# Optimization experiments

Hardware: AMD Instinct MI355X
Metric: run time of the kernel (lower is better)

The kernel has to match this reference:

```python
import jax, jax.numpy as jnp
import numpy as np

EPS_NORM = 1e-12
BN_EPS = 1e-5

def _l2norm(x, axis=-1):
    n = jnp.sqrt(jnp.sum(x * x, axis=axis, keepdims=True))
    return x / jnp.maximum(n, EPS_NORM)

def setup_inputs() -> dict:
    key = jax.random.key(0)
    ks = jax.random.split(key, 16)
    B, C, H, W, K = 32, 256, 64, 64, 5
    supp_feat = jax.random.normal(ks[0], (B, C, H, W), dtype=jnp.float32)
    supp_mask = (jax.random.uniform(ks[1], (B, 1, H, W)) > 0.5).astype(jnp.float32)
    part_queries = 0.02 * jax.random.normal(ks[2], (1, K, C), dtype=jnp.float32)
    temperature = jnp.array([0.1], dtype=jnp.float32)
    margin = jnp.array([0.15], dtype=jnp.float32)
    q_w = jax.random.normal(ks[3], (C, C), dtype=jnp.float32) / np.sqrt(C)  # 1x1 conv, no bias
    bn_w = 1.0 + 0.1 * jax.random.normal(ks[4], (C,), dtype=jnp.float32)
    bn_b = 0.1 * jax.random.normal(ks[5], (C,), dtype=jnp.float32)
    bn_mean = 0.1 * jax.random.normal(ks[6], (C,), dtype=jnp.float32)
    bn_var = 0.5 + jax.random.uniform(ks[7], (C,), dtype=jnp.float32)
    k_w = jax.random.normal(ks[8], (C, C), dtype=jnp.float32) / np.sqrt(C)
    k_b = 0.01 * jax.random.normal(ks[9], (C,), dtype=jnp.float32)
    v_w = jax.random.normal(ks[10], (C, C), dtype=jnp.float32) / np.sqrt(C)
    v_b = 0.01 * jax.random.normal(ks[11], (C,), dtype=jnp.float32)
    out_w = jax.random.normal(ks[12], (C, C), dtype=jnp.float32) / np.sqrt(C)
    out_b = 0.01 * jax.random.normal(ks[13], (C,), dtype=jnp.float32)
    gamma = jnp.array([0.1], dtype=jnp.float32)  # nonzero so the refine branch contributes
    return {"supp_feat": supp_feat, "supp_mask": supp_mask, "part_queries": part_queries,
            "temperature": temperature, "margin": margin, "q_w": q_w, "bn_w": bn_w,
            "bn_b": bn_b, "bn_mean": bn_mean, "bn_var": bn_var, "k_w": k_w, "k_b": k_b,
            "v_w": v_w, "v_b": v_b, "out_w": out_w, "out_b": out_b, "gamma": gamma}

def reference(supp_feat, supp_mask, part_queries, temperature, margin, q_w, bn_w, bn_b,
              bn_mean, bn_var, k_w, k_b, v_w, v_b, out_w, out_b, gamma):
    B, C, H, W = supp_feat.shape
    K = part_queries.shape[1]
    flat_mask = supp_mask.reshape(B, -1)                       # [B, HW]
    flat_feat = jnp.swapaxes(supp_feat.reshape(B, C, -1), 1, 2)  # [B, HW, C]
    queries_norm = _l2norm(part_queries)[0]                    # [K, C]
    feat_norm = _l2norm(flat_feat)                             # [B, HW, C]
    temp = jnp.maximum(temperature, 0.01)[0]
    sim = jnp.einsum('kc,bnc->bkn', queries_norm, feat_norm) / temp  # [B, K, HW]
    sim = jnp.where(flat_mask[:, None, :] > 0, sim, -jnp.inf)
    attn = jnp.nan_to_num(jax.nn.softmax(sim, axis=-1), nan=0.0)
    part_tokens = jnp.einsum('bkn,bnc->bkc', attn, flat_feat)  # [B, K, C]
    # diversity loss
    nt = _l2norm(part_tokens)
    cos = jnp.einsum('bkc,bjc->bkj', nt, nt) * (1.0 - jnp.eye(K, dtype=supp_feat.dtype))
    m = jnp.clip(margin, 0.0, 0.5)[0]
    div_loss = jnp.maximum(cos - m, 0.0).sum() / (B * K * (K - 1) + 1e-5)
    # refine attention
    q = jnp.einsum('oc,bchw->bohw', q_w, supp_feat)            # 1x1 conv, no bias
    scale = bn_w / jnp.sqrt(bn_var + BN_EPS)
    q = q * scale[None, :, None, None] + (bn_b - bn_mean * scale)[None, :, None, None]
    Q = jnp.swapaxes(q.reshape(B, C, -1), 1, 2)                # [B, HW, C]
    Kt = part_tokens @ k_w.T + k_b                             # [B, K, C]
    Vt = part_tokens @ v_w.T + v_b
    refine = jax.nn.softmax(jnp.einsum('bnc,bkc->bnk', Q, Kt) / (C ** 0.5), axis=-1)
    attn_out = jnp.einsum('bnk,bkc->bnc', refine, Vt)          # [B, HW, C]
    attn_out = jnp.swapaxes(attn_out, 1, 2).reshape(B, C, H, W)
    attn_out = jnp.einsum('oc,bchw->bohw', out_w, attn_out) + out_b[None, :, None, None]
    enhanced = supp_feat + gamma[0] * attn_out
    return (enhanced, div_loss, part_tokens)
```

## Files before the change

kernel.cpp:

```cpp
#include <hip/hip_runtime.h>
#include <hip/hip_bf16.h>
#include <math.h>

#define B_  32
#define C_  256
#define HW_ 4096
#define K_  5
#define P_  128
#define NT_ 32
#define PS_ 68
#define FS_ 66

typedef __hip_bfloat16 bf16;
typedef unsigned int u32;
typedef __attribute__((ext_vector_type(8))) short bf16x8;
typedef __attribute__((ext_vector_type(4))) float f32x4;

template<bool BF>
__device__ inline float LD(const void* p, size_t i) {
    if (BF) return __bfloat162float(((const bf16*)p)[i]);
    return ((const float*)p)[i];
}
template<bool BF>
__device__ inline void ST(void* p, size_t i, float v) {
    if (BF) ((bf16*)p)[i] = __float2bfloat16(v);
    else    ((float*)p)[i] = v;
}
template<bool BF>
__device__ inline float4 LD4(const void* p, size_t i) {
    if (BF) {
        ushort4 u = *(const ushort4*)((const unsigned short*)p + i);
        float4 r;
        r.x = __uint_as_float(((u32)u.x) << 16);
        r.y = __uint_as_float(((u32)u.y) << 16);
        r.z = __uint_as_float(((u32)u.z) << 16);
        r.w = __uint_as_float(((u32)u.w) << 16);
        return r;
    }
    return *(const float4*)((const float*)p + i);
}
__device__ inline u32 packbf2(float a, float b) {
    bf16 x = __float2bfloat16(a), y = __float2bfloat16(b);
    return (((u32)*(unsigned short*)&y) << 16) | (u32)(*(unsigned short*)&x);
}
__device__ inline float lo16f(u32 u) { return __uint_as_float(u << 16); }
__device__ inline float hi16f(u32 u) { return __uint_as_float(u & 0xffff0000u); }

__device__ int detect_bf(const void* feat, int* cntL) {
    int t = threadIdx.x;
    if (t == 0) *cntL = 0;
    __syncthreads();
    const unsigned short* u = (const unsigned short*)feat;
    float v = __uint_as_float(((u32)u[t]) << 16);
    float a = fabsf(v);
    int local = (a >= 1e-4f && a <= 100.f) ? 1 : 0;
    for (int o = 32; o > 0; o >>= 1) local += __shfl_down(local, o, 64);
    if ((t & 63) == 0) atomicAdd(cntL, local);
    __syncthreads();
    return (*cntL > (int)(3u * blockDim.x / 4u)) ? 1 : 0;
}

__device__ inline float blk_sum(float v, float* sh) {
    for (int o = 32; o > 0; o >>= 1) v += __shfl_down(v, o, 64);
    int w = threadIdx.x >> 6;
    __syncthreads();
    if ((threadIdx.x & 63) == 0) sh[w] = v;
    __syncthreads();
    return sh[0] + sh[1] + sh[2] + sh[3];
}

template<bool BF>
__device__ void simpt_body(const void* feat, const void* mask, const void* temp,
                           const void* pq, float* ptp, float* mz, float* smem) {
    u32*   featB = (u32*)smem;
    float* red   = smem + 17408;
    u32*   wB    = (u32*)red;
    float* qL    = smem + 17408 + 1536;
    float* simL  = qL;
    float* sc    = qL + 1280;
    int t = threadIdx.x, lane = t & 63, q = t >> 6;
    int b = blockIdx.y, tile = blockIdx.x;

    if (q < K_) {
        float4 v = LD4<BF>(pq, (size_t)q * C_ + lane * 4);
        float ss = v.x * v.x + v.y * v.y + v.z * v.z + v.w * v.w;
        for (int o = 32; o > 0; o >>= 1) ss += __shfl_xor(ss, o, 64);
        float inv = 1.0f / fmaxf(sqrtf(ss), 1e-12f);
        *(float4*)(qL + q * C_ + lane * 4) =
            make_float4(v.x * inv, v.y * inv, v.z * inv, v.w * inv);
    }
    if (t == 0) sc[0] = 1.0f / fmaxf(LD<BF>(temp, 0), 0.01f);
    __syncthreads();

    int c0 = q * 32, half = lane >> 5, lm = lane & 31;
    float sa[4] = {0.f, 0.f, 0.f, 0.f};
    float da[K_][4];
    #pragma unroll
    for (int k = 0; k < K_; k++)
        #pragma unroll
        for (int i = 0; i < 4; i++) da[k][i] = 0.f;
    size_t gbase = (size_t)b * C_ * HW_ + (size_t)tile * P_ + lm * 4;
    #pragma unroll
    for (int j = 0; j < 16; j++) {
        int c = c0 + 2 * j + half;
        float4 f = LD4<BF>(feat, gbase + (size_t)c * HW_);
        sa[0] += f.x * f.x; sa[1] += f.y * f.y; sa[2] += f.z * f.z; sa[3] += f.w * f.w;
        #pragma unroll
        for (int k = 0; k < K_; k++) {
            float qv = qL[k * C_ + c];
            da[k][0] += f.x * qv; da[k][1] += f.y * qv;
            da[k][2] += f.z * qv; da[k][3] += f.w * qv;
        }
        *(uint2*)&featB[c * PS_ + 2 * lm] =
            make_uint2(packbf2(f.x, f.y), packbf2(f.z, f.w));
    }
    #pragma unroll
    for (int i = 0; i < 4; i++) sa[i] += __shfl_down(sa[i], 32, 64);
    #pragma unroll
    for (int k = 0; k < K_; k++)
        #pragma unroll
        for (int i = 0; i < 4; i++) da[k][i] += __shfl_down(da[k][i], 32, 64);

    float4 mpre = make_float4(0.f, 0.f, 0.f, 0.f);
    if (t < 160) mpre = LD4<BF>(mask, (size_t)b * HW_ + tile * P_ + (t & 31) * 4);
    float tinv = sc[0];
    #pragma unroll
    for (int r = 0; r < 4; r++) {
        if (lane < 32) {
            red[0 * 256 + q * 32 + lane] = sa[r];
            #pragma unroll
            for (int k = 0; k < K_; k++) red[(1 + k) * 256 + q * 32 + lane] = da[k][r];
        }
        __syncthreads();
        if (t < 160) {
            int kk = t >> 5, m = t & 31, n = 4 * m + r;
            float ssum = 0.f, dsum = 0.f;
            #pragma unroll
            for (int g = 0; g < 8; g++) {
                ssum += red[0 * 256 + g * 32 + m];
                dsum += red[(1 + kk) * 256 + g * 32 + m];
            }
            float mval = (r == 0) ? mpre.x : (r == 1) ? mpre.y : (r == 2) ? mpre.z : mpre.w;
            simL[kk * P_ + n] = (mval > 0.f)
                ? dsum * (tinv / fmaxf(sqrtf(ssum), 1e-12f)) : -INFINITY;
        }
        __syncthreads();
    }

    if (q < K_) {
        float s0 = simL[q * P_ + 2 * lane], s1 = simL[q * P_ + 2 * lane + 1];
        float m = fmaxf(s0, s1);
        for (int o = 32; o > 0; o >>= 1) m = fmaxf(m, __shfl_xor(m, o, 64));
        float e0 = (s0 == -INFINITY) ? 0.f : __expf(s0 - m);
        float e1 = (s1 == -INFINITY) ? 0.f : __expf(s1 - m);
        float z = e0 + e1;
        for (int o = 32; o > 0; o >>= 1) z += __shfl_xor(z, o, 64);
        wB[q * PS_ + lane] = packbf2(e0, e1);
        if (lane == 0) {
            size_t mzb = ((size_t)(b * NT_ + tile) * K_ + q) * 2;
            mz[mzb] = m; mz[mzb + 1] = z;
        }
    }
    __syncthreads();

    int r16 = lane & 15, g = lane >> 4;
    size_t pb = (size_t)(b * NT_ + tile) * (K_ * C_);
    #pragma unroll
    for (int sub = 0; sub < 2; sub++) {
        int ctile = q * 32 + sub * 16;
        f32x4 acc = {0.f, 0.f, 0.f, 0.f};
        #pragma unroll
        for (int s = 0; s < 4; s++) {
            bf16x8 a = *(const bf16x8*)(featB + (ctile + r16) * PS_ + 16 * s + 4 * g);
            bf16x8 bb = *(const bf16x8*)(wB + r16 * PS_ + 16 * s + 4 * g);
            acc = __builtin_amdgcn_mfma_f32_16x16x32_bf16(a, bb, acc, 0, 0, 0);
        }
        if (r16 < K_) {
            #pragma unroll
            for (int r = 0; r < 4; r++)
                ptp[pb + (size_t)r16 * C_ + ctile + 4 * g + r] = acc[r];
        }
    }
}
__global__ __launch_bounds__(512, 4) void k_simpt(const void* feat, const void* mask,
                                                  const void* temp, const void* pq,
                                                  float* ptp, float* mz) {
    __shared__ __attribute__((aligned(16))) float smem[20232];
    __shared__ int cnt;
    int flg = detect_bf(feat, &cnt);
    if (flg) simpt_body<true >(feat, mask, temp, pq, ptp, mz, smem);
    else     simpt_body<false>(feat, mask, temp, pq, ptp, mz, smem);
}

__device__ inline float merge_one(const float* ptp, const float* mz,
                                  int b, int kk, int c) {
    float M = -INFINITY;
    #pragma unroll 8
    for (int tl = 0; tl < NT_; tl++)
        M = fmaxf(M, mz[((size_t)(b * NT_ + tl) * K_ + kk) * 2]);
    float Zs = 0.f, acc = 0.f;
    #pragma unroll 8
    for (int tl = 0; tl < NT_; tl++) {
        size_t mzb = ((size_t)(b * NT_ + tl) * K_ + kk) * 2;
        float m_t = mz[mzb], z_t = mz[mzb + 1];
        float s = (m_t == -INFINITY) ? 0.f : __expf(m_t - M);
        Zs += z_t * s;
        acc += ptp[(size_t)(b * NT_ + tl) * (K_ * C_) + kk * C_ + c] * s;
    }
    return (Zs > 0.f) ? acc / Zs : 0.f;
}
template<bool BF>
__device__ void prep_part(const void* qw, const void* kw, const void* kb,
                          const void* vw, const void* vb, const void* ow,
                          const void* bnw, const void* bnb, const void* bnm,
                          const void* bnv, float ptv, int bk,
                          float* W2, float* b2, float* OV, float* pt, float* smem) {
    float* ptL = smem;
    float* KtL = smem + 256;
    float* VtL = smem + 512;
    float* sh  = smem + 768;
    int t = threadIdx.x;
    ptL[t] = ptv;
    pt[(size_t)bk * C_ + t] = ptv;
    __syncthreads();
    float kt = LD<BF>(kb, t), vt = LD<BF>(vb, t);
    for (int c = 0; c < C_; c += 4) {
        float4 p4 = *(float4*)(ptL + c);
        float4 kw4 = LD4<BF>(kw, (size_t)t * C_ + c);
        float4 vw4 = LD4<BF>(vw, (size_t)t * C_ + c);
        kt += kw4.x * p4.x + kw4.y * p4.y + kw4.z * p4.z + kw4.w * p4.w;
        vt += vw4.x * p4.x + vw4.y * p4.y + vw4.z * p4.z + vw4.w * p4.w;
    }
    float scale = LD<BF>(bnw, t) * rsqrtf(LD<BF>(bnv, t) + 1e-5f);
    float shift = LD<BF>(bnb, t) - LD<BF>(bnm, t) * scale;
    KtL[t] = kt * scale;
    VtL[t] = vt;
    float bpart = kt * shift;
    __syncthreads();
    float ov = 0;
    for (int c = 0; c < C_; c += 4) {
        float4 v4 = *(float4*)(VtL + c);
        float4 ow4 = LD4<BF>(ow, (size_t)t * C_ + c);
        ov += ow4.x * v4.x + ow4.y * v4.y + ow4.z * v4.z + ow4.w * v4.w;
    }
    OV[(size_t)bk * C_ + t] = ov;
    float w2 = 0;
    for (int o = 0; o < C_; o++) w2 += KtL[o] * LD<BF>(qw, (size_t)o * C_ + t);
    W2[(size_t)bk * C_ + t] = w2 * (1.0f / 16.0f);
    float bs = blk_sum(bpart, sh);
    if (t == 0) b2[bk] = bs * (1.0f / 16.0f);
}
template<bool BF>
__device__ void div_part(const float* ptp, const float* mz, const void* margin,
                         float* divpart, float* smem) {
    float* ptL = smem;
    float* rn  = smem + K_ * C_;
    float* sh  = rn + 8;
    int b = blockIdx.x - B_ * K_, t = threadIdx.x;
    for (int kk = 0; kk < K_; kk++) ptL[kk * C_ + t] = merge_one(ptp, mz, b, kk, t);
    __syncthreads();
    for (int k = 0; k < K_; k++) {
        float v = ptL[k * C_ + t];
        float s = blk_sum(v * v, sh);
        if (t == 0) rn[k] = 1.0f / fmaxf(sqrtf(s), 1e-12f);
    }
    __syncthreads();
    float m = LD<BF>(margin, 0);
    m = fminf(fmaxf(m, 0.f), 0.5f);
    int p = t >> 3, g = t & 7;
    float contrib = 0.f;
    if (p < K_ * K_) {
        int k = p / K_, j = p % K_;
        float d = 0;
        for (int c = g; c < C_; c += 8) d += ptL[k * C_ + c] * ptL[j * C_ + c];
        d += __shfl_down(d, 4, 8);
        d += __shfl_down(d, 2, 8);
        d += __shfl_down(d, 1, 8);
        if (g == 0 && k != j) contrib = fmaxf(d * rn[k] * rn[j] - m, 0.f);
    }
    float s = blk_sum(contrib, sh);
    if (t == 0) divpart[b] = s;
}
template<bool BF>
__device__ void mergeprep_body(const void* qw, const void* kw, const void* kb,
                               const void* vw, const void* vb, const void* ow,
                               const void* bnw, const void* bnb, const void* bnm,
                               const void* bnv, const void* margin,
                               const float* ptp, const float* mz,
                               float* W2, float* b2, float* OV, float* pt,
                               float* divpart, float* smem) {
    int bid = blockIdx.x, t = threadIdx.x;
    if (bid < B_ * K_) {
        int b = bid / K_, kk = bid % K_;
        float ptv = merge_one(ptp, mz, b, kk, t);
        prep_part<BF>(qw, kw, kb, vw, vb, ow, bnw, bnb, bnm, bnv,
                      ptv, bid, W2, b2, OV, pt, smem);
    } else {
        div_part<BF>(ptp, mz, margin, divpart, smem);
    }
}
__global__ void k_mergeprep(const void* feat, const void* qw, const void* kw,
                            const void* kb, const void* vw, const void* vb,
                            const void* ow, const void* bnw, const void* bnb,
                            const void* bnm, const void* bnv, const void* margin,
                            const float* ptp, const float* mz,
                            float* W2, float* b2, float* OV, float* pt, float* divpart) {
    __shared__ __attribute__((aligned(16))) float smem[K_ * C_ + 16];
    __shared__ int cnt;
    int flg = detect_bf(feat, &cnt);
    if (flg) mergeprep_body<true >(qw, kw, kb, vw, vb, ow, bnw, bnb, bnm, bnv, margin,
                                   ptp, mz, W2, b2, OV, pt, divpart, smem);
    else     mergeprep_body<false>(qw, kw, kb, vw, vb, ow, bnw, bnb, bnm, bnv, margin,
                                   ptp, mz, W2, b2, OV, pt, divpart, smem);
}

template<bool BF>
__device__ void fin_body(const void* feat, const void* outb, const void* gamma,
                         const float* W2, const float* b2, const float* OV,
                         const float* pt, const float* divpart,
                         void* dout, float* smem) {
    u32*   featU = (u32*)smem;
    u32*   OVp8  = featU + 256 * FS_;
    u32*   eT8   = OVp8 + 1024;
    u32*   zb    = eT8 + 512;
    float* pool  = (float*)(zb + 4);
    u32*   W2p   = (u32*)pool;
    float* red   = pool;
    float* b2L   = pool + 1280;
    int t = threadIdx.x, lane = t & 63, q = t >> 6;
    int b = blockIdx.y, tile = blockIdx.x;

    float g0 = LD<BF>(gamma, 0);
    for (int i = t; i < 640; i += 512) {
        W2p[i] = packbf2(W2[(size_t)b * 1280 + 2 * i], W2[(size_t)b * 1280 + 2 * i + 1]);
    }
    if (t < 256) {
        float o0 = OV[(size_t)b * 1280 + 0 * C_ + t] * g0;
        float o1 = OV[(size_t)b * 1280 + 1 * C_ + t] * g0;
        float o2 = OV[(size_t)b * 1280 + 2 * C_ + t] * g0;
        float o3 = OV[(size_t)b * 1280 + 3 * C_ + t] * g0;
        float o4 = OV[(size_t)b * 1280 + 4 * C_ + t] * g0;
        float obv = LD<BF>(outb, t) * g0;
        OVp8[t * 4 + 0] = packbf2(o0, o1);
        OVp8[t * 4 + 1] = packbf2(o2, o3);
        OVp8[t * 4 + 2] = packbf2(o4, obv);
        OVp8[t * 4 + 3] = 0u;
    }
    if (t < 4) zb[t] = 0u;
    if (t < K_) b2L[t] = b2[b * K_ + t];
    __syncthreads();

    int c0 = q * 32, half = lane >> 5, lm = lane & 31;
    size_t gbase = (size_t)b * C_ * HW_ + (size_t)tile * P_ + lm * 4;
    float la[K_][4];
    #pragma unroll
    for (int k = 0; k < K_; k++)
        #pragma unroll
        for (int i = 0; i < 4; i++) la[k][i] = 0.f;
    #pragma unroll
    for (int j = 0; j < 16; j++) {
        int c = c0 + 2 * j + half;
        float4 f = LD4<BF>(feat, gbase + (size_t)c * HW_);
        #pragma unroll
        for (int k = 0; k < K_; k++) {
            u32 u = W2p[k * 128 + (c >> 1)];
            float wv = half ? hi16f(u) : lo16f(u);
            la[k][0] += f.x * wv; la[k][1] += f.y * wv;
            la[k][2] += f.z * wv; la[k][3] += f.w * wv;
        }
        *(uint2*)&featU[c * FS_ + 2 * lm] =
            make_uint2(packbf2(f.x, f.y), packbf2(f.z, f.w));
    }
    #pragma unroll
    for (int k = 0; k < K_; k++)
        #pragma unroll
        for (int i = 0; i < 4; i++) la[k][i] += __shfl_down(la[k][i], 32, 64);
    __syncthreads();

    #pragma unroll
    for (int r = 0; r < 4; r++) {
        if (lane < 32) {
            #pragma unroll
            for (int k = 0; k < K_; k++) red[k * 256 + q * 32 + lane] = la[k][r];
        }
        __syncthreads();
        if (t < 32) {
            int n = 4 * t + r;
            float lg[K_];
            #pragma unroll
            for (int k = 0; k < K_; k++) {
                float s = b2L[k];
                #pragma unroll
                for (int gg = 0; gg < 8; gg++) s += red[k * 256 + gg * 32 + t];
                lg[k] = s;
            }
            float mx = fmaxf(fmaxf(fmaxf(lg[0], lg[1]), fmaxf(lg[2], lg[3])), lg[4]);
            float e0 = __expf(lg[0] - mx), e1 = __expf(lg[1] - mx),
                  e2 = __expf(lg[2] - mx), e3 = __expf(lg[3] - mx),
                  e4 = __expf(lg[4] - mx);
            float inv = 1.0f / (e0 + e1 + e2 + e3 + e4);
            eT8[n * 4 + 0] = packbf2(e0 * inv, e1 * inv);
            eT8[n * 4 + 1] = packbf2(e2 * inv, e3 * inv);
            eT8[n * 4 + 2] = packbf2(e4 * inv, 1.0f);
            eT8[n * 4 + 3] = 0u;
        }
        __syncthreads();
    }

    int r16 = lane & 15, gg = lane >> 4;
    const bf16x8 zfrag = *(const bf16x8*)zb;
    size_t base = (size_t)b * C_ * HW_ + (size_t)tile * P_;
    #pragma unroll
    for (int ct = 0; ct < 2; ct++) {
        int ctile = (q * 2 + ct) * 16;
        bf16x8 a = (gg == 0) ? *(const bf16x8*)(OVp8 + (ctile + r16) * 4) : zfrag;
        #pragma unroll
        for (int pt8 = 0; pt8 < 8; pt8++) {
            int ptile = pt8 * 16;
            bf16x8 bb = (gg == 0) ? *(const bf16x8*)(eT8 + (ptile + r16) * 4) : zfrag;
            f32x4 acc = {0.f, 0.f, 0.f, 0.f};
            acc = __builtin_amdgcn_mfma_f32_16x16x32_bf16(a, bb, acc, 0, 0, 0);
            int p = ptile + r16;
            #pragma unroll
            for (int r = 0; r < 4; r++) {
                int c = ctile + 4 * gg + r;
                u32 w = featU[c * FS_ + (p >> 1)];
                float f = (p & 1) ? hi16f(w) : lo16f(w);
                ST<BF>(dout, base + (size_t)c * HW_ + p, f + acc[r]);
            }
        }
    }
    if (b == 0) {
        const size_t enh = (size_t)B_ * C_ * HW_;
        for (int i = blockIdx.x * 512 + t; i < B_ * K_ * C_; i += NT_ * 512)
            ST<BF>(dout, enh + 1 + i, pt[i]);
        if (blockIdx.x == 0 && t == 0) {
            float s = 0;
            for (int bb2 = 0; bb2 < B_; bb2++) s += divpart[bb2];
            ST<BF>(dout, enh, s / (640.0f + 1e-5f));
        }
    }
}
__global__ __launch_bounds__(512, 4) void k_fin(const void* feat, const void* outb,
                                                const void* gamma, const float* W2,
                                                const float* b2, const float* OV,
                                                const float* pt, const float* divpart,
                                                void* dout) {
    __shared__ __attribute__((aligned(16))) float smem[19728];
    __shared__ int cnt;
    int flg = detect_bf(feat, &cnt);
    if (flg) fin_body<true >(feat, outb, gamma, W2, b2, OV, pt, divpart, dout, smem);
    else     fin_body<false>(feat, outb, gamma, W2, b2, OV, pt, divpart, dout, smem);
}

extern "C" void kernel_launch(void* const* d_in, const int* in_sizes, int n_in,
                              void* d_out, int out_size, void* d_ws, size_t ws_size,
                              hipStream_t stream) {
    const void* feat = d_in[0];
    const void* mask = d_in[1];
    const void* pq   = d_in[2];
    const void* temp = d_in[3];
    const void* marg = d_in[4];
    const void* qw   = d_in[5];
    const void* bnw  = d_in[6];
    const void* bnb  = d_in[7];
    const void* bnm  = d_in[8];
    const void* bnv  = d_in[9];
    const void* kw   = d_in[10];
    const void* kb   = d_in[11];
    const void* vw   = d_in[12];
    const void* vb   = d_in[13];
    const void* ow   = d_in[14];
    const void* ob   = d_in[15];
    const void* gm   = d_in[16];

    float* ws  = (float*)d_ws;
    float* ptp = ws;
    float* mz  = ptp + (size_t)B_ * NT_ * K_ * C_;
    float* pt  = mz  + (size_t)B_ * NT_ * K_ * 2;
    float* W2  = pt  + B_ * K_ * C_;
    float* b2  = W2  + B_ * K_ * C_;
    float* OV  = b2  + B_ * K_;
    float* dvp = OV  + B_ * K_ * C_;

    hipLaunchKernelGGL(k_simpt, dim3(NT_, B_), dim3(512), 0, stream,
                       feat, mask, temp, pq, ptp, mz);
    hipLaunchKernelGGL(k_mergeprep, dim3(B_ * K_ + B_), dim3(256), 0, stream,
                       feat, qw, kw, kb, vw, vb, ow, bnw, bnb, bnm, bnv, marg,
                       ptp, mz, W2, b2, OV, pt, dvp);
    hipLaunchKernelGGL(k_fin, dim3(NT_, B_), dim3(512), 0, stream,
                       feat, ob, gm, W2, b2, OV, pt, dvp, d_out);
}
```

Measured before the change: 131.3 us.

## Remap thread-to-pixel layout so channel reductions use wave shuffles instead of LDS

In both the similarity/part-token kernel and the final kernel, each wave now owns 16 pixels, with 16 lanes covering channel subsets. Per-pixel channel reductions become in-wave xor shuffles, replacing the LDS scatter/gather loop that needed eight block barriers. The softmax max is combined across waves through a small shared array, and the exp/sum runs in registers. Shared memory footprint also shrinks. The trade-off is more shuffle instructions and a global read pattern that may coalesce less well across 16-channel strides.

```diff
diff --git a/kernel.cpp b/kernel.cpp
--- a/kernel.cpp
+++ b/kernel.cpp
@@ -73,12 +73,13 @@
 __device__ void simpt_body(const void* feat, const void* mask, const void* temp,
                            const void* pq, float* ptp, float* mz, float* smem) {
     u32*   featB = (u32*)smem;
-    float* red   = smem + 17408;
-    u32*   wB    = (u32*)red;
-    float* qL    = smem + 17408 + 1536;
-    float* simL  = qL;
-    float* sc    = qL + 1280;
+    u32*   wB    = featB + 256 * PS_;
+    float* qL    = (float*)(wB + 16 * PS_);
+    float* mL    = qL + 1280;
+    float* zL    = mL + 40;
+    float* sc    = zL + 40;
     int t = threadIdx.x, lane = t & 63, q = t >> 6;
+    int r16 = lane & 15, g = lane >> 4;
     int b = blockIdx.y, tile = blockIdx.x;
 
     if (q < K_) {
@@ -92,17 +93,17 @@
     if (t == 0) sc[0] = 1.0f / fmaxf(LD<BF>(temp, 0), 0.01f);
     __syncthreads();
 
-    int c0 = q * 32, half = lane >> 5, lm = lane & 31;
+    int pbase = tile * P_ + q * 16 + 4 * g;
+    size_t gbase = (size_t)b * C_ * HW_ + pbase;
     float sa[4] = {0.f, 0.f, 0.f, 0.f};
     float da[K_][4];
     #pragma unroll
     for (int k = 0; k < K_; k++)
         #pragma unroll
         for (int i = 0; i < 4; i++) da[k][i] = 0.f;
-    size_t gbase = (size_t)b * C_ * HW_ + (size_t)tile * P_ + lm * 4;
     #pragma unroll
     for (int j = 0; j < 16; j++) {
-        int c = c0 + 2 * j + half;
+        int c = j * 16 + r16;
         float4 f = LD4<BF>(feat, gbase + (size_t)c * HW_);
         sa[0] += f.x * f.x; sa[1] += f.y * f.y; sa[2] += f.z * f.z; sa[3] += f.w * f.w;
         #pragma unroll
@@ -111,59 +112,73 @@
             da[k][0] += f.x * qv; da[k][1] += f.y * qv;
             da[k][2] += f.z * qv; da[k][3] += f.w * qv;
         }
-        *(uint2*)&featB[c * PS_ + 2 * lm] =
+        *(uint2*)&featB[c * PS_ + 8 * q + 2 * g] =
             make_uint2(packbf2(f.x, f.y), packbf2(f.z, f.w));
     }
     #pragma unroll
-    for (int i = 0; i < 4; i++) sa[i] += __shfl_down(sa[i], 32, 64);
-    #pragma unroll
-    for (int k = 0; k < K_; k++)
-        #pragma unroll
-        for (int i = 0; i < 4; i++) da[k][i] += __shfl_down(da[k][i], 32, 64);
-
-    float4 mpre = make_float4(0.f, 0.f, 0.f, 0.f);
-    if (t < 160) mpre = LD4<BF>(mask, (size_t)b * HW_ + tile * P_ + (t & 31) * 4);
+    for (int o = 1; o <= 8; o <<= 1) {
+        #pragma unroll
+        for (int i = 0; i < 4; i++) sa[i] += __shfl_xor(sa[i], o, 64);
+        #pragma unroll
+        for (int k = 0; k < K_; k++)
+            #pragma unroll
+            for (int i = 0; i < 4; i++) da[k][i] += __shfl_xor(da[k][i], o, 64);
+    }
     float tinv = sc[0];
-    #pragma unroll
-    for (int r = 0; r < 4; r++) {
-        if (lane < 32) {
-            red[0 * 256 + q * 32 + lane] = sa[r];
-            #pragma unroll
-            for (int k = 0; k < K_; k++) red[(1 + k) * 256 + q * 32 + lane] = da[k][r];
-        }
-        __syncthreads();
-        if (t < 160) {
-            int kk = t >> 5, m = t & 31, n = 4 * m + r;
-            float ssum = 0.f, dsum = 0.f;
-            #pragma unroll
-            for (int g = 0; g < 8; g++) {
-                ssum += red[0 * 256 + g * 32 + m];
-                dsum += red[(1 + kk) * 256 + g * 32 + m];
-            }
-            float mval = (r == 0) ? mpre.x : (r == 1) ? mpre.y : (r == 2) ? mpre.z : mpre.w;
-            simL[kk * P_ + n] = (mval > 0.f)
-                ? dsum * (tinv / fmaxf(sqrtf(ssum), 1e-12f)) : -INFINITY;
-        }
-        __syncthreads();
-    }
-
-    if (q < K_) {
-        float s0 = simL[q * P_ + 2 * lane], s1 = simL[q * P_ + 2 * lane + 1];
-        float m = fmaxf(s0, s1);
-        for (int o = 32; o > 0; o >>= 1) m = fmaxf(m, __shfl_xor(m, o, 64));
-        float e0 = (s0 == -INFINITY) ? 0.f : __expf(s0 - m);
-        float e1 = (s1 == -INFINITY) ? 0.f : __expf(s1 - m);
-        float z = e0 + e1;
-        for (int o = 32; o > 0; o >>= 1) z += __shfl_xor(z, o, 64);
-        wB[q * PS_ + lane] = packbf2(e0, e1);
-        if (lane == 0) {
-            size_t mzb = ((size_t)(b * NT_ + tile) * K_ + q) * 2;
-            mz[mzb] = m; mz[mzb + 1] = z;
-        }
-    }
-    __syncthreads();
-
-    int r16 = lane & 15, g = lane >> 4;
+    float4 m4 = LD4<BF>(mask, (size_t)b * HW_ + pbase);
+    float mv[4] = {m4.x, m4.y, m4.z, m4.w};
+    float sv[K_][4];
+    #pragma unroll
+    for (int i = 0; i < 4; i++) {
+        float inv = tinv / fmaxf(sqrtf(sa[i]), 1e-12f);
+        #pragma unroll
+        for (int k = 0; k < K_; k++)
+            sv[k][i] = (mv[i] > 0.f) ? da[k][i] * inv : -INFINITY;
+    }
+    float mw[K_];
+    #pragma unroll
+    for (int k = 0; k < K_; k++) {
+        float m = fmaxf(fmaxf(sv[k][0], sv[k][1]), fmaxf(sv[k][2], sv[k][3]));
+        m = fmaxf(m, __shfl_xor(m, 16, 64));
+        m = fmaxf(m, __shfl_xor(m, 32, 64));
+        mw[k] = m;
+    }
+    if (lane == 0) {
+        #pragma unroll
+        for (int k = 0; k < K_; k++) mL[q * K_ + k] = mw[k];
+    }
+    __syncthreads();
+
+    float M[K_];
+    #pragma unroll
+    for (int k = 0; k < K_; k++) {
+        float m = mL[k];
+        #pragma unroll
+        for (int l = 1; l < 8; l++) m = fmaxf(m, mL[l * K_ + k]);
+        M[k] = m;
+    }
+    float e[K_][4];
+    #pragma unroll
+    for (int k = 0; k < K_; k++) {
+        float z = 0.f;
+        #pragma unroll
+        for (int i = 0; i < 4; i++) {
+            e[k][i] = (sv[k][i] == -INFINITY) ? 0.f : __expf(sv[k][i] - M[k]);
+            z += e[k][i];
+        }
+        z += __shfl_xor(z, 16, 64);
+        z += __shfl_xor(z, 32, 64);
+        if (lane == 0) zL[q * K_ + k] = z;
+    }
+    if (r16 < K_) {
+        #pragma unroll
+        for (int k = 0; k < K_; k++)
+            if (r16 == k)
+                *(uint2*)&wB[k * PS_ + 8 * q + 2 * g] =
+                    make_uint2(packbf2(e[k][0], e[k][1]), packbf2(e[k][2], e[k][3]));
+    }
+    __syncthreads();
+
     size_t pb = (size_t)(b * NT_ + tile) * (K_ * C_);
     #pragma unroll
     for (int sub = 0; sub < 2; sub++) {
@@ -181,11 +196,18 @@
                 ptp[pb + (size_t)r16 * C_ + ctile + 4 * g + r] = acc[r];
         }
     }
+    if (q < K_ && lane == 0) {
+        float zt = 0.f;
+        #pragma unroll
+        for (int l = 0; l < 8; l++) zt += zL[l * K_ + q];
+        size_t mzb = ((size_t)(b * NT_ + tile) * K_ + q) * 2;
+        mz[mzb] = M[q]; mz[mzb + 1] = zt;
+    }
 }
 __global__ __launch_bounds__(512, 4) void k_simpt(const void* feat, const void* mask,
                                                   const void* temp, const void* pq,
                                                   float* ptp, float* mz) {
-    __shared__ __attribute__((aligned(16))) float smem[20232];
+    __shared__ __attribute__((aligned(16))) float smem[19872];
     __shared__ int cnt;
     int flg = detect_bf(feat, &cnt);
     if (flg) simpt_body<true >(feat, mask, temp, pq, ptp, mz, smem);
@@ -323,11 +345,10 @@
     u32*   OVp8  = featU + 256 * FS_;
     u32*   eT8   = OVp8 + 1024;
     u32*   zb    = eT8 + 512;
-    float* pool  = (float*)(zb + 4);
-    u32*   W2p   = (u32*)pool;
-    float* red   = pool;
-    float* b2L   = pool + 1280;
+    u32*   W2p   = zb + 4;
+    float* b2L   = (float*)(W2p + 640);
     int t = threadIdx.x, lane = t & 63, q = t >> 6;
+    int r16 = lane & 15, g = lane >> 4;
     int b = blockIdx.y, tile = blockIdx.x;
 
     float g0 = LD<BF>(gamma, 0);
@@ -350,8 +371,8 @@
     if (t < K_) b2L[t] = b2[b * K_ + t];
     __syncthreads();
 
-    int c0 = q * 32, half = lane >> 5, lm = lane & 31;
-    size_t gbase = (size_t)b * C_ * HW_ + (size_t)tile * P_ + lm * 4;
+    int pbase = tile * P_ + q * 16 + 4 * g;
+    size_t gbase = (size_t)b * C_ * HW_ + pbase;
     float la[K_][4];
     #pragma unroll
     for (int k = 0; k < K_; k++)
@@ -359,57 +380,48 @@
         for (int i = 0; i < 4; i++) la[k][i] = 0.f;
     #pragma unroll
     for (int j = 0; j < 16; j++) {
-        int c = c0 + 2 * j + half;
+        int c = j * 16 + r16;
         float4 f = LD4<BF>(feat, gbase + (size_t)c * HW_);
         #pragma unroll
         for (int k = 0; k < K_; k++) {
             u32 u = W2p[k * 128 + (c >> 1)];
-            float wv = half ? hi16f(u) : lo16f(u);
+            float wv = (r16 & 1) ? hi16f(u) : lo16f(u);
             la[k][0] += f.x * wv; la[k][1] += f.y * wv;
             la[k][2] += f.z * wv; la[k][3] += f.w * wv;
         }
-        *(uint2*)&featU[c * FS_ + 2 * lm] =
+        *(uint2*)&featU[c * FS_ + 8 * q + 2 * g] =
             make_uint2(packbf2(f.x, f.y), packbf2(f.z, f.w));
     }
     #pragma unroll
-    for (int k = 0; k < K_; k++)
-        #pragma unroll
-        for (int i = 0; i < 4; i++) la[k][i] += __shfl_down(la[k][i], 32, 64);
-    __syncthreads();
-
-    #pragma unroll
-    for (int r = 0; r < 4; r++) {
-        if (lane < 32) {
+    for (int o = 1; o <= 8; o <<= 1)
+        #pragma unroll
+        for (int k = 0; k < K_; k++)
             #pragma unroll
-            for (int k = 0; k < K_; k++) red[k * 256 + q * 32 + lane] = la[k][r];
-        }
-        __syncthreads();
-        if (t < 32) {
-            int n = 4 * t + r;
-            float lg[K_];
-            #pragma unroll
-            for (int k = 0; k < K_; k++) {
-                float s = b2L[k];
-                #pragma unroll
-                for (int gg = 0; gg < 8; gg++) s += red[k * 256 + gg * 32 + t];
-                lg[k] = s;
-            }
-            float mx = fmaxf(fmaxf(fmaxf(lg[0], lg[1]), fmaxf(lg[2], lg[3])), lg[4]);
-            float e0 = __expf(lg[0] - mx), e1 = __expf(lg[1] - mx),
-                  e2 = __expf(lg[2] - mx), e3 = __expf(lg[3] - mx),
-                  e4 = __expf(lg[4] - mx);
-            float inv = 1.0f / (e0 + e1 + e2 + e3 + e4);
-            eT8[n * 4 + 0] = packbf2(e0 * inv, e1 * inv);
-            eT8[n * 4 + 1] = packbf2(e2 * inv, e3 * inv);
-            eT8[n * 4 + 2] = packbf2(e4 * inv, 1.0f);
-            eT8[n * 4 + 3] = 0u;
-        }
-        __syncthreads();
-    }
-
-    int r16 = lane & 15, gg = lane >> 4;
+            for (int i = 0; i < 4; i++) la[k][i] += __shfl_xor(la[k][i], o, 64);
+
+    #pragma unroll
+    for (int i = 0; i < 4; i++) {
+        float lg[K_];
+        #pragma unroll
+        for (int k = 0; k < K_; k++) lg[k] = la[k][i] + b2L[k];
+        float mx = fmaxf(fmaxf(fmaxf(lg[0], lg[1]), fmaxf(lg[2], lg[3])), lg[4]);
+        float e0 = __expf(lg[0] - mx), e1 = __expf(lg[1] - mx),
+              e2 = __expf(lg[2] - mx), e3 = __expf(lg[3] - mx),
+              e4 = __expf(lg[4] - mx);
+        float inv = 1.0f / (e0 + e1 + e2 + e3 + e4);
+        if (r16 == i) {
+            int p = q * 16 + 4 * g + i;
+            eT8[p * 4 + 0] = packbf2(e0 * inv, e1 * inv);
+            eT8[p * 4 + 1] = packbf2(e2 * inv, e3 * inv);
+            eT8[p * 4 + 2] = packbf2(e4 * inv, 1.0f);
+            eT8[p * 4 + 3] = 0u;
+        }
+    }
+    __syncthreads();
+
     const bf16x8 zfrag = *(const bf16x8*)zb;
     size_t base = (size_t)b * C_ * HW_ + (size_t)tile * P_;
+    int gg = lane >> 4;
     #pragma unroll
     for (int ct = 0; ct < 2; ct++) {
         int ctile = (q * 2 + ct) * 16;
@@ -446,7 +458,7 @@
                                                 const float* b2, const float* OV,
                                                 const float* pt, const float* divpart,
                                                 void* dout) {
-    __shared__ __attribute__((aligned(16))) float smem[19728];
+    __shared__ __attribute__((aligned(16))) float smem[19100];
     __shared__ int cnt;
     int flg = detect_bf(feat, &cnt);
     if (flg) fin_body<true >(feat, outb, gamma, W2, b2, OV, pt, divpart, dout, smem);
```

Result: no change. 133.5 us (+1.7%).
